# Performance work log

Measured on AMD Instinct MI355X. Metric: run time of the kernel, lower is better.

The kernel has to match this reference:

```python
import jax, jax.numpy as jnp
import numpy as np

# module config (mirrors init_kwargs)
D_MODEL = 1024
N_HEADS = 16
HEAD_DIM = D_MODEL // N_HEADS
WINDOW = 512
PREFIX = 16
B = 2
S = 4096  # divisible by WINDOW; S > WINDOW + PREFIX -> chunked windowed path


def setup_inputs() -> dict:
    key = jax.random.key(0)
    k1, k2, k3 = jax.random.split(key, 3)
    x = jax.random.normal(k1, (B, S, D_MODEL), dtype=jnp.float32)
    w_qkv = jax.random.normal(k2, (3 * D_MODEL, D_MODEL), dtype=jnp.float32) * 0.02
    w_out = jax.random.normal(k3, (D_MODEL, D_MODEL), dtype=jnp.float32) * 0.02
    return {"x": x, "w_qkv": w_qkv, "w_out": w_out}


def _windowed_global_attention(q, k, v):
    """q,k,v: [B,H,S,Dh]. Causal sliding-window (WINDOW) + global prefix (PREFIX) attention.
    Exactly matches torch's chunked SDPA: for query chunk starting at q_start, allowed keys are
    k_pos < PREFIX (causal) plus local keys in (q_pos-WINDOW, q_pos] with k_pos >= PREFIX."""
    Bb, H, S_, Dh = q.shape
    W, P = WINDOW, PREFIX
    C = S_ // W  # number of query chunks
    scale = 1.0 / np.sqrt(Dh).astype(np.float32)

    qc = q.reshape(Bb, H, C, W, Dh)  # [B,H,C,W,Dh]
    # pad W zero-keys at front so every chunk gathers a uniform 2W-key local tail
    kp = jnp.pad(k, ((0, 0), (0, 0), (W, 0), (0, 0)))
    vp = jnp.pad(v, ((0, 0), (0, 0), (W, 0), (0, 0)))
    tail_idx = jnp.arange(C)[:, None] * W + jnp.arange(2 * W)[None, :]  # [C,2W] (padded coords)
    kt = kp[:, :, tail_idx, :]  # [B,H,C,2W,Dh]
    vt = vp[:, :, tail_idx, :]
    kg = k[:, :, :P, :]  # global prefix keys [B,H,P,Dh]
    vg = v[:, :, :P, :]

    sg = jnp.einsum('bhcqd,bhkd->bhcqk', qc, kg) * scale   # [B,H,C,W,P]
    st = jnp.einsum('bhcqd,bhckd->bhcqk', qc, kt) * scale  # [B,H,C,W,2W]

    q_pos = jnp.arange(C)[:, None] * W + jnp.arange(W)[None, :]          # [C,W]
    kt_pos = jnp.arange(C)[:, None] * W - W + jnp.arange(2 * W)[None, :]  # [C,2W]
    # global prefix: causal only
    mg = jnp.arange(P)[None, None, :] <= q_pos[:, :, None]                # [C,W,P]
    # local tail: causal & within window & not already covered by global prefix (and not padding)
    diff = q_pos[:, :, None] - kt_pos[:, None, :]                          # [C,W,2W]
    mt = (diff >= 0) & (diff < W) & (kt_pos[:, None, :] >= P)

    neg = jnp.asarray(-1e9, sg.dtype)
    scores = jnp.concatenate([
        jnp.where(mg[None, None], sg, neg),
        jnp.where(mt[None, None], st, neg),
    ], axis=-1)  # [B,H,C,W,P+2W]
    attn = jax.nn.softmax(scores, axis=-1)

    vcat = jnp.concatenate([
        jnp.broadcast_to(vg[:, :, None], (Bb, H, C, P, Dh)), vt
    ], axis=3)  # [B,H,C,P+2W,Dh]
    out = jnp.einsum('bhcqk,bhckd->bhcqd', attn, vcat)
    return out.reshape(Bb, H, S_, Dh)


def reference(x, w_qkv, w_out):
    Bb, S_, Dm = x.shape
    qkv = x @ w_qkv.T                      # [B,S,3*Dm]
    q, k, v = jnp.split(qkv, 3, axis=-1)
    def heads(t):
        return t.reshape(Bb, S_, N_HEADS, HEAD_DIM).transpose(0, 2, 1, 3)
    q, k, v = heads(q), heads(k), heads(v)  # [B,H,S,Dh]
    o = _windowed_global_attention(q, k, v)
    o = o.transpose(0, 2, 1, 3).reshape(Bb, S_, Dm)
    return o @ w_out.T
```

## Files before the change

kernel.cpp:

```cpp
#include <hip/hip_runtime.h>
#include <hip/hip_bf16.h>

#define AS1 __attribute__((address_space(1)))
#define AS3 __attribute__((address_space(3)))

typedef unsigned short u16;
typedef short bf16x8 __attribute__((ext_vector_type(8)));
typedef unsigned short u16x8 __attribute__((ext_vector_type(8)));
typedef float f32x4 __attribute__((ext_vector_type(4)));

#define MFMA16 __builtin_amdgcn_mfma_f32_16x16x32_bf16


__device__ __forceinline__ u16 f2bf(float f) {
  union { float f; unsigned u; } c; c.f = f;
  unsigned u = c.u;
  u = u + 0x7fffu + ((u >> 16) & 1u);
  return (u16)(u >> 16);
}

__device__ __forceinline__ void gl_lds16(const void* g, void* l) {
  __builtin_amdgcn_global_load_lds((const AS1 void*)g, (AS3 void*)l, 16, 0, 0);
}

union fpu { float f; unsigned u; };


__global__ void cast_all_kernel(const float* __restrict__ x,
                                const float* __restrict__ wqkv,
                                const float* __restrict__ wout,
                                u16* __restrict__ ws) {
  int i = blockIdx.x * blockDim.x + threadIdx.x;
  const float4* src;
  int rel;
  size_t matbase;
  if (i < 2097152)      { src = (const float4*)x + i;                rel = i;           matbase = 0; }
  else if (i < 2883584) { src = (const float4*)wqkv + (i - 2097152); rel = i - 2097152; matbase = 8388608; }
  else                  { src = (const float4*)wout + (i - 2883584); rel = i - 2883584; matbase = 11534336; }
  float4 f = *src;
  ushort4 o;
  o.x = f2bf(f.x); o.y = f2bf(f.y); o.z = f2bf(f.z); o.w = f2bf(f.w);
  int fe  = rel * 4;
  int row = fe >> 10, c = fe & 1023;
  int newc = (c & ~63) | (((((c >> 3) ^ row) & 7) << 3)) | (c & 7);
  ((ushort4*)ws)[(matbase + (size_t)row * 1024 + newc) >> 2] = o;
}


template<int EPI>
__global__ __launch_bounds__(256) void gemm_bt(
    const u16* __restrict__ A, const u16* __restrict__ Bm,
    float* __restrict__ Cf,
    u16* __restrict__ qd, u16* __restrict__ kd, u16* __restrict__ vd,
    int M, int N, int K)
{
  __shared__ u16 As[128 * 64];
  __shared__ u16 Bs[128 * 64];

  const int tid  = threadIdx.x;
  const int wave = tid >> 6, lane = tid & 63;
  const int quad = lane >> 4, l16 = lane & 15;
  const int bm = blockIdx.y * 128, bn = blockIdx.x * 128;
  const int wm = (wave >> 1) * 64, wn = (wave & 1) * 64;

  f32x4 acc[4][4] = {};

  const int srow = wave * 32 + (lane >> 3);
  const int scol = (lane & 7) * 8;

  for (int kt = 0; kt < K; kt += 64) {
    __syncthreads();
    #pragma unroll
    for (int i = 0; i < 4; ++i) {
      gl_lds16(&A[(size_t)(bm + srow + i * 8) * K + kt + scol], &As[(wave * 32 + i * 8) * 64]);
      gl_lds16(&Bm[(size_t)(bn + srow + i * 8) * K + kt + scol], &Bs[(wave * 32 + i * 8) * 64]);
    }
    __syncthreads();
    #pragma unroll
    for (int kk = 0; kk < 64; kk += 32) {
      bf16x8 af[4], bb[4];
      #pragma unroll
      for (int i = 0; i < 4; ++i) {
        int row = wm + i * 16 + l16;
        af[i] = *(const bf16x8*)&As[row * 64 + (((((kk >> 3) + quad) ^ row) & 7) << 3)];
      }
      #pragma unroll
      for (int j = 0; j < 4; ++j) {
        int row = wn + j * 16 + l16;
        bb[j] = *(const bf16x8*)&Bs[row * 64 + (((((kk >> 3) + quad) ^ row) & 7) << 3)];
      }
      #pragma unroll
      for (int i = 0; i < 4; ++i)
        #pragma unroll
        for (int j = 0; j < 4; ++j)
          acc[i][j] = MFMA16(af[i], bb[j], acc[i][j], 0, 0, 0);
    }
  }

  #pragma unroll
  for (int i = 0; i < 4; ++i) {
    #pragma unroll
    for (int j = 0; j < 4; ++j) {
      #pragma unroll
      for (int r = 0; r < 4; ++r) {
        int m = bm + wm + i * 16 + quad * 4 + r;
        int n = bn + wn + j * 16 + l16;
        float val = acc[i][j][r];
        if (EPI == 0) {
          Cf[(size_t)m * N + n] = val;
        } else {
          int part = n >> 10, rem = n & 1023;
          int h = rem >> 6, d = rem & 63;
          int b = m >> 12, s = m & 4095;
          if (part == 0) val *= 0.1803368801111244f;
          u16* dst = (part == 0) ? qd : (part == 1) ? kd : vd;
          dst[((size_t)((b * 16 + h) * 4096 + s)) * 64 + d] = f2bf(val);
        }
      }
    }
  }
}


__global__ __launch_bounds__(256) void transpose_v(const u16* __restrict__ vb,
                                                   u16* __restrict__ vt) {
  __shared__ u16 Lt[64 * 72];
  const int tid = threadIdx.x, bid = blockIdx.x;
  const int bh = bid & 31, st = (bid >> 5) << 6;
  const size_t base = (size_t)bh << 18;
  #pragma unroll
  for (int c = 0; c < 2; ++c) {
    int idx = tid * 8 + c * 2048;
    int row = idx >> 6, col = idx & 63;
    u16x8 vv = *(const u16x8*)&vb[base + (size_t)(st + row) * 64 + col];
    #pragma unroll
    for (int s = 0; s < 8; ++s) Lt[(col + s) * 72 + row] = vv[s];
  }
  __syncthreads();
  #pragma unroll
  for (int c = 0; c < 2; ++c) {
    int d = (tid >> 3) + c * 32;
    int sg = (tid & 7) * 8;
    u16x8 o;
    #pragma unroll
    for (int s = 0; s < 8; ++s) o[s] = Lt[d * 72 + sg + s];
    *(u16x8*)&vt[base + (size_t)d * 4096 + st + sg] = o;
  }
}


__global__ __launch_bounds__(64) void attn_kernel(
    const u16* __restrict__ qb, const u16* __restrict__ kb,
    const u16* __restrict__ vt, u16* __restrict__ ob)
{
  __shared__ u16 Ps[32 * 64];

  const int lane = threadIdx.x;
  const int quad = lane >> 4, l16 = lane & 15;
  const int bid  = blockIdx.x;
  const int bh   = bid & 31;
  const int t0   = (bid >> 5) << 5;
  const size_t base = (size_t)bh << 18;

  bf16x8 bq[2][2];
  #pragma unroll
  for (int i = 0; i < 2; ++i) {
    const u16* qrow = qb + base + (size_t)(t0 + i * 16 + l16) * 64;
    bq[i][0] = *(const bf16x8*)(qrow + quad * 8);
    bq[i][1] = *(const bf16x8*)(qrow + 32 + quad * 8);
  }

  f32x4 oacc[2][4] = {};
  f32x4 lacc[2] = {};
  bf16x8 ones;
  #pragma unroll
  for (int s = 0; s < 8; ++s) ones[s] = (short)0x3F80;

  const int lo = max(0, t0 - 511) >> 6;
  const int hi = (t0 + 31) >> 6;

  auto loadK = [&](int kb0, bf16x8 (&kf)[4][2]) {
    #pragma unroll
    for (int j = 0; j < 4; ++j) {
      const u16* krow = kb + base + (size_t)(kb0 + j * 16 + l16) * 64;
      kf[j][0] = *(const bf16x8*)(krow + quad * 8);
      kf[j][1] = *(const bf16x8*)(krow + 32 + quad * 8);
    }
  };

  bf16x8 ka[4][2], kbuf2[4][2];

  {
    const u16* krow = kb + base + (size_t)l16 * 64;
    bf16x8 pk0 = *(const bf16x8*)(krow + quad * 8);
    bf16x8 pk1 = *(const bf16x8*)(krow + 32 + quad * 8);
    loadK(lo << 6, ka);

    #pragma unroll
    for (int i = 0; i < 2; ++i) {
      f32x4 t4 = {};
      t4 = MFMA16(pk0, bq[i][0], t4, 0, 0, 0);
      t4 = MFMA16(pk1, bq[i][1], t4, 0, 0, 0);
      int row = i * 16 + l16;
      int qpos = t0 + row;
      fpu p[4];
      #pragma unroll
      for (int r = 0; r < 4; ++r) {
        int kpos = quad * 4 + r;
        p[r].f = exp2f(kpos <= qpos ? t4[r] : -1e30f);
      }
      uint2 w;
      w.x = (p[1].u & 0xffff0000u) | (p[0].u >> 16);
      w.y = (p[3].u & 0xffff0000u) | (p[2].u >> 16);
      *(uint2*)&Ps[row * 64 + ((quad ^ l16) & 15) * 4] = w;
      uint2 z = {0u, 0u};
      *(uint2*)&Ps[row * 64 + (((4 + quad) ^ l16) & 15) * 4] = z;
    }
    #pragma unroll
    for (int i = 0; i < 2; ++i) {
      int row = i * 16 + l16;
      uint2 r0 = *(uint2*)&Ps[row * 64 + (((2 * quad) ^ l16) & 15) * 4];
      uint2 r1 = *(uint2*)&Ps[row * 64 + (((2 * quad + 1) ^ l16) & 15) * 4];
      union { uint4 u; bf16x8 v; } cc; cc.u = make_uint4(r0.x, r0.y, r1.x, r1.y);
      bf16x8 ap = cc.v;
      lacc[i] = MFMA16(ap, ones, lacc[i], 0, 0, 0);
      #pragma unroll
      for (int jd = 0; jd < 4; ++jd) {
        bf16x8 bv = *(const bf16x8*)&vt[base + (size_t)(jd * 16 + l16) * 4096 + quad * 8];
        oacc[i][jd] = MFMA16(ap, bv, oacc[i][jd], 0, 0, 0);
      }
    }
  }

  auto tilec = [&](int kb0, bf16x8 (&kf)[4][2]) {
    const bool full = (kb0 >= 16) && (kb0 + 63 <= t0) && (kb0 >= t0 + 31 - 511);
    #pragma unroll
    for (int j = 0; j < 4; ++j) {
      #pragma unroll
      for (int i = 0; i < 2; ++i) {
        f32x4 t4 = {};
        t4 = MFMA16(kf[j][0], bq[i][0], t4, 0, 0, 0);
        t4 = MFMA16(kf[j][1], bq[i][1], t4, 0, 0, 0);
        int row = i * 16 + l16;
        int qpos = t0 + row;
        fpu p[4];
        #pragma unroll
        for (int r = 0; r < 4; ++r) {
          float v = t4[r];
          if (!full) {
            int kpos = kb0 + j * 16 + quad * 4 + r;
            int diff = qpos - kpos;
            bool ok = (diff >= 0) && (diff < 512) && (kpos >= 16);
            v = ok ? v : -1e30f;
          }
          p[r].f = exp2f(v);
        }
        uint2 w;
        w.x = (p[1].u & 0xffff0000u) | (p[0].u >> 16);
        w.y = (p[3].u & 0xffff0000u) | (p[2].u >> 16);
        *(uint2*)&Ps[row * 64 + (((j * 4 + quad) ^ l16) & 15) * 4] = w;
      }
    }
    #pragma unroll
    for (int i = 0; i < 2; ++i) {
      int row = i * 16 + l16;
      #pragma unroll
      for (int h = 0; h < 2; ++h) {
        int g0 = h * 8 + 2 * quad;
        uint2 r0 = *(uint2*)&Ps[row * 64 + ((g0 ^ l16) & 15) * 4];
        uint2 r1 = *(uint2*)&Ps[row * 64 + (((g0 + 1) ^ l16) & 15) * 4];
        union { uint4 u; bf16x8 v; } cc; cc.u = make_uint4(r0.x, r0.y, r1.x, r1.y);
        bf16x8 ap = cc.v;
        lacc[i] = MFMA16(ap, ones, lacc[i], 0, 0, 0);
        #pragma unroll
        for (int jd = 0; jd < 4; ++jd) {
          bf16x8 bv = *(const bf16x8*)&vt[base + (size_t)(jd * 16 + l16) * 4096 + kb0 + h * 32 + quad * 8];
          oacc[i][jd] = MFMA16(ap, bv, oacc[i][jd], 0, 0, 0);
        }
      }
    }
  };

  for (int t = lo; t <= hi; t += 2) {
    if (t + 1 <= hi) loadK((t + 1) << 6, kbuf2);
    tilec(t << 6, ka);
    if (t + 1 <= hi) {
      if (t + 2 <= hi) loadK((t + 2) << 6, ka);
      tilec((t + 1) << 6, kbuf2);
    }
  }

  const int b = bh >> 4, h = bh & 15;
  #pragma unroll
  for (int i = 0; i < 2; ++i) {
    #pragma unroll
    for (int r = 0; r < 4; ++r) {
      float inv = 1.f / lacc[i][r];
      int srow = t0 + i * 16 + quad * 4 + r;
      size_t rowoff = ((size_t)(b * 4096 + srow)) * 1024 + h * 64;
      #pragma unroll
      for (int jd = 0; jd < 4; ++jd) {
        int g = ((jd * 2 + (l16 >> 3)) ^ srow) & 7;
        ob[rowoff + (g << 3) + (l16 & 7)] = f2bf(oacc[i][jd][r] * inv);
      }
    }
  }
}


extern "C" void kernel_launch(void* const* d_in, const int* in_sizes, int n_in,
                              void* d_out, int out_size, void* d_ws, size_t ws_size,
                              hipStream_t stream) {
  const float* x    = (const float*)d_in[0];
  const float* wqkv = (const float*)d_in[1];
  const float* wout = (const float*)d_in[2];
  float* out = (float*)d_out;

  u16* ws    = (u16*)d_ws;
  u16* xb    = ws;
  u16* wqkvb = xb + (size_t)8192 * 1024;
  u16* woutb = wqkvb + (size_t)3072 * 1024;
  u16* qbuf  = woutb + (size_t)1024 * 1024;
  u16* kbuf  = qbuf + (size_t)8388608;
  u16* vbuf  = kbuf + (size_t)8388608;
  u16* vtb   = vbuf + (size_t)8388608;
  u16* obuf  = xb;

  cast_all_kernel<<<12288, 256, 0, stream>>>(x, wqkv, wout, ws);

  gemm_bt<1><<<dim3(24, 64), 256, 0, stream>>>(xb, wqkvb, nullptr, qbuf, kbuf, vbuf,
                                               8192, 3072, 1024);
  transpose_v<<<2048, 256, 0, stream>>>(vbuf, vtb);
  attn_kernel<<<4096, 64, 0, stream>>>(qbuf, kbuf, vtb, obuf);
  gemm_bt<0><<<dim3(8, 64), 256, 0, stream>>>(obuf, woutb, out, nullptr, nullptr, nullptr,
                                              8192, 1024, 1024);
}
```

Baseline: 265.2 us.

## Pack four attention waves per block and prefetch V/K tiles in registers

The attention kernel now runs four independent waves per 256-thread block, each handling its own 32-query tile with a private LDS slice, in place of one 64-thread wave per block. The K/V loop is restructured to a single-tile loop that preloads the V fragments at the top of each iteration and prefetches the next K tile after the QK MFMAs, using precomputed pointers. Exp2 uses the hardware builtin, and bf16 packing uses a single perm instruction. This is meant to cut per-block launch overhead and hide global-load latency, at the cost of higher register pressure under the launch_bounds(256,3) occupancy target.

```diff
diff --git a/kernel.cpp b/kernel.cpp
--- a/kernel.cpp
+++ b/kernel.cpp
@@ -19,11 +19,22 @@
   return (u16)(u >> 16);
 }
 
+__device__ __forceinline__ float fexp2(float x) {
+#if __has_builtin(__builtin_amdgcn_exp2f)
+  return __builtin_amdgcn_exp2f(x);
+#else
+  return exp2f(x);
+#endif
+}
+
+__device__ __forceinline__ unsigned pack_bf(float a, float b) {
+  union { float f; unsigned u; } ua, ub; ua.f = a; ub.f = b;
+  return __builtin_amdgcn_perm(ub.u, ua.u, 0x07060302u);
+}
+
 __device__ __forceinline__ void gl_lds16(const void* g, void* l) {
   __builtin_amdgcn_global_load_lds((const AS1 void*)g, (AS3 void*)l, 16, 0, 0);
 }
-
-union fpu { float f; unsigned u; };
 
 
 __global__ void cast_all_kernel(const float* __restrict__ x,
@@ -149,26 +160,46 @@
 }
 
 
-__global__ __launch_bounds__(64) void attn_kernel(
+__global__ __launch_bounds__(256, 3) void attn_kernel(
     const u16* __restrict__ qb, const u16* __restrict__ kb,
     const u16* __restrict__ vt, u16* __restrict__ ob)
 {
-  __shared__ u16 Ps[32 * 64];
-
-  const int lane = threadIdx.x;
+  __shared__ u16 Ps[4][32 * 64];
+
+  const int tid  = threadIdx.x;
+  const int wave = tid >> 6;
+  const int lane = tid & 63;
   const int quad = lane >> 4, l16 = lane & 15;
   const int bid  = blockIdx.x;
   const int bh   = bid & 31;
-  const int t0   = (bid >> 5) << 5;
+  const int t0   = (((bid >> 5) << 2) | wave) << 5;
   const size_t base = (size_t)bh << 18;
-
-  bf16x8 bq[2][2];
-  #pragma unroll
-  for (int i = 0; i < 2; ++i) {
-    const u16* qrow = qb + base + (size_t)(t0 + i * 16 + l16) * 64;
-    bq[i][0] = *(const bf16x8*)(qrow + quad * 8);
-    bq[i][1] = *(const bf16x8*)(qrow + 32 + quad * 8);
-  }
+  u16* __restrict__ ps = &Ps[wave][0];
+
+  const int l64 = l16 * 64 + quad * 8;
+
+  const u16* qp = qb + base + (size_t)t0 * 64 + l64;
+  bf16x8 bq00 = *(const bf16x8*)(qp);
+  bf16x8 bq01 = *(const bf16x8*)(qp + 32);
+  bf16x8 bq10 = *(const bf16x8*)(qp + 1024);
+  bf16x8 bq11 = *(const bf16x8*)(qp + 1056);
+
+  const int lo = max(0, t0 - 511) >> 6;
+  const int hi = (t0 + 31) >> 6;
+
+  const u16* kp0 = kb + base + (size_t)(lo << 6) * 64 + l64;
+  const u16* kp2 = kp0 + 2048;
+  const u16* vq  = vt + base + (size_t)l16 * 4096 + quad * 8;
+  const u16* vp0 = vq + (lo << 6);
+  const u16* vp1 = vp0 + 65536;
+  const u16* vp2 = vp1 + 65536;
+  const u16* vp3 = vp2 + 65536;
+
+  bf16x8 kf[4][2];
+  kf[0][0] = *(const bf16x8*)(kp0);        kf[0][1] = *(const bf16x8*)(kp0 + 32);
+  kf[1][0] = *(const bf16x8*)(kp0 + 1024); kf[1][1] = *(const bf16x8*)(kp0 + 1056);
+  kf[2][0] = *(const bf16x8*)(kp2);        kf[2][1] = *(const bf16x8*)(kp2 + 32);
+  kf[3][0] = *(const bf16x8*)(kp2 + 1024); kf[3][1] = *(const bf16x8*)(kp2 + 1056);
 
   f32x4 oacc[2][4] = {};
   f32x4 lacc[2] = {};
@@ -176,118 +207,124 @@
   #pragma unroll
   for (int s = 0; s < 8; ++s) ones[s] = (short)0x3F80;
 
-  const int lo = max(0, t0 - 511) >> 6;
-  const int hi = (t0 + 31) >> 6;
-
-  auto loadK = [&](int kb0, bf16x8 (&kf)[4][2]) {
-    #pragma unroll
-    for (int j = 0; j < 4; ++j) {
-      const u16* krow = kb + base + (size_t)(kb0 + j * 16 + l16) * 64;
-      kf[j][0] = *(const bf16x8*)(krow + quad * 8);
-      kf[j][1] = *(const bf16x8*)(krow + 32 + quad * 8);
-    }
-  };
-
-  bf16x8 ka[4][2], kbuf2[4][2];
-
   {
-    const u16* krow = kb + base + (size_t)l16 * 64;
-    bf16x8 pk0 = *(const bf16x8*)(krow + quad * 8);
-    bf16x8 pk1 = *(const bf16x8*)(krow + 32 + quad * 8);
-    loadK(lo << 6, ka);
+    const u16* kpre = kb + base + l64;
+    bf16x8 pk0 = *(const bf16x8*)(kpre);
+    bf16x8 pk1 = *(const bf16x8*)(kpre + 32);
+    bf16x8 pv[4];
+    pv[0] = *(const bf16x8*)(vq);
+    pv[1] = *(const bf16x8*)(vq + 65536);
+    pv[2] = *(const bf16x8*)(vq + 131072);
+    pv[3] = *(const bf16x8*)(vq + 196608);
 
     #pragma unroll
     for (int i = 0; i < 2; ++i) {
       f32x4 t4 = {};
-      t4 = MFMA16(pk0, bq[i][0], t4, 0, 0, 0);
-      t4 = MFMA16(pk1, bq[i][1], t4, 0, 0, 0);
+      t4 = MFMA16(pk0, i ? bq10 : bq00, t4, 0, 0, 0);
+      t4 = MFMA16(pk1, i ? bq11 : bq01, t4, 0, 0, 0);
       int row = i * 16 + l16;
       int qpos = t0 + row;
-      fpu p[4];
+      float p[4];
       #pragma unroll
       for (int r = 0; r < 4; ++r) {
         int kpos = quad * 4 + r;
-        p[r].f = exp2f(kpos <= qpos ? t4[r] : -1e30f);
+        p[r] = fexp2(kpos <= qpos ? t4[r] : -1e30f);
       }
       uint2 w;
-      w.x = (p[1].u & 0xffff0000u) | (p[0].u >> 16);
-      w.y = (p[3].u & 0xffff0000u) | (p[2].u >> 16);
-      *(uint2*)&Ps[row * 64 + ((quad ^ l16) & 15) * 4] = w;
-      uint2 z = {0u, 0u};
-      *(uint2*)&Ps[row * 64 + (((4 + quad) ^ l16) & 15) * 4] = z;
+      w.x = pack_bf(p[0], p[1]);
+      w.y = pack_bf(p[2], p[3]);
+      *(uint2*)&ps[row * 64 + ((quad ^ l16) & 15) * 4] = w;
+      uint2 z; z.x = 0u; z.y = 0u;
+      *(uint2*)&ps[row * 64 + (((4 + quad) ^ l16) & 15) * 4] = z;
     }
     #pragma unroll
     for (int i = 0; i < 2; ++i) {
       int row = i * 16 + l16;
-      uint2 r0 = *(uint2*)&Ps[row * 64 + (((2 * quad) ^ l16) & 15) * 4];
-      uint2 r1 = *(uint2*)&Ps[row * 64 + (((2 * quad + 1) ^ l16) & 15) * 4];
+      uint2 r0 = *(uint2*)&ps[row * 64 + (((2 * quad) ^ l16) & 15) * 4];
+      uint2 r1 = *(uint2*)&ps[row * 64 + (((2 * quad + 1) ^ l16) & 15) * 4];
       union { uint4 u; bf16x8 v; } cc; cc.u = make_uint4(r0.x, r0.y, r1.x, r1.y);
       bf16x8 ap = cc.v;
       lacc[i] = MFMA16(ap, ones, lacc[i], 0, 0, 0);
       #pragma unroll
-      for (int jd = 0; jd < 4; ++jd) {
-        bf16x8 bv = *(const bf16x8*)&vt[base + (size_t)(jd * 16 + l16) * 4096 + quad * 8];
-        oacc[i][jd] = MFMA16(ap, bv, oacc[i][jd], 0, 0, 0);
-      }
-    }
-  }
-
-  auto tilec = [&](int kb0, bf16x8 (&kf)[4][2]) {
+      for (int jd = 0; jd < 4; ++jd)
+        oacc[i][jd] = MFMA16(ap, pv[jd], oacc[i][jd], 0, 0, 0);
+    }
+  }
+
+  for (int t = lo; t <= hi; ++t) {
+    const int kb0 = t << 6;
     const bool full = (kb0 >= 16) && (kb0 + 63 <= t0) && (kb0 >= t0 + 31 - 511);
+
+    bf16x8 bv[2][4];
+    bv[0][0] = *(const bf16x8*)(vp0);  bv[1][0] = *(const bf16x8*)(vp0 + 32);
+    bv[0][1] = *(const bf16x8*)(vp1);  bv[1][1] = *(const bf16x8*)(vp1 + 32);
+    bv[0][2] = *(const bf16x8*)(vp2);  bv[1][2] = *(const bf16x8*)(vp2 + 32);
+    bv[0][3] = *(const bf16x8*)(vp3);  bv[1][3] = *(const bf16x8*)(vp3 + 32);
+
+    f32x4 sc[4][2];
     #pragma unroll
     for (int j = 0; j < 4; ++j) {
       #pragma unroll
       for (int i = 0; i < 2; ++i) {
         f32x4 t4 = {};
-        t4 = MFMA16(kf[j][0], bq[i][0], t4, 0, 0, 0);
-        t4 = MFMA16(kf[j][1], bq[i][1], t4, 0, 0, 0);
+        t4 = MFMA16(kf[j][0], i ? bq10 : bq00, t4, 0, 0, 0);
+        t4 = MFMA16(kf[j][1], i ? bq11 : bq01, t4, 0, 0, 0);
+        sc[j][i] = t4;
+      }
+    }
+
+    if (t < hi) {
+      kp0 += 4096; kp2 += 4096;
+      kf[0][0] = *(const bf16x8*)(kp0);        kf[0][1] = *(const bf16x8*)(kp0 + 32);
+      kf[1][0] = *(const bf16x8*)(kp0 + 1024); kf[1][1] = *(const bf16x8*)(kp0 + 1056);
+      kf[2][0] = *(const bf16x8*)(kp2);        kf[2][1] = *(const bf16x8*)(kp2 + 32);
+      kf[3][0] = *(const bf16x8*)(kp2 + 1024); kf[3][1] = *(const bf16x8*)(kp2 + 1056);
+    }
+
+    #pragma unroll
+    for (int j = 0; j < 4; ++j) {
+      #pragma unroll
+      for (int i = 0; i < 2; ++i) {
         int row = i * 16 + l16;
-        int qpos = t0 + row;
-        fpu p[4];
-        #pragma unroll
-        for (int r = 0; r < 4; ++r) {
-          float v = t4[r];
-          if (!full) {
+        float p[4];
+        if (full) {
+          #pragma unroll
+          for (int r = 0; r < 4; ++r) p[r] = fexp2(sc[j][i][r]);
+        } else {
+          int qpos = t0 + row;
+          #pragma unroll
+          for (int r = 0; r < 4; ++r) {
             int kpos = kb0 + j * 16 + quad * 4 + r;
             int diff = qpos - kpos;
             bool ok = (diff >= 0) && (diff < 512) && (kpos >= 16);
-            v = ok ? v : -1e30f;
+            p[r] = fexp2(ok ? sc[j][i][r] : -1e30f);
           }
-          p[r].f = exp2f(v);
         }
         uint2 w;
-        w.x = (p[1].u & 0xffff0000u) | (p[0].u >> 16);
-        w.y = (p[3].u & 0xffff0000u) | (p[2].u >> 16);
-        *(uint2*)&Ps[row * 64 + (((j * 4 + quad) ^ l16) & 15) * 4] = w;
-      }
-    }
+        w.x = pack_bf(p[0], p[1]);
+        w.y = pack_bf(p[2], p[3]);
+        *(uint2*)&ps[row * 64 + (((j * 4 + quad) ^ l16) & 15) * 4] = w;
+      }
+    }
+
     #pragma unroll
     for (int i = 0; i < 2; ++i) {
       int row = i * 16 + l16;
       #pragma unroll
       for (int h = 0; h < 2; ++h) {
         int g0 = h * 8 + 2 * quad;
-        uint2 r0 = *(uint2*)&Ps[row * 64 + ((g0 ^ l16) & 15) * 4];
-        uint2 r1 = *(uint2*)&Ps[row * 64 + (((g0 + 1) ^ l16) & 15) * 4];
+        uint2 r0 = *(uint2*)&ps[row * 64 + ((g0 ^ l16) & 15) * 4];
+        uint2 r1 = *(uint2*)&ps[row * 64 + (((g0 + 1) ^ l16) & 15) * 4];
         union { uint4 u; bf16x8 v; } cc; cc.u = make_uint4(r0.x, r0.y, r1.x, r1.y);
         bf16x8 ap = cc.v;
         lacc[i] = MFMA16(ap, ones, lacc[i], 0, 0, 0);
         #pragma unroll
-        for (int jd = 0; jd < 4; ++jd) {
-          bf16x8 bv = *(const bf16x8*)&vt[base + (size_t)(jd * 16 + l16) * 4096 + kb0 + h * 32 + quad * 8];
-          oacc[i][jd] = MFMA16(ap, bv, oacc[i][jd], 0, 0, 0);
-        }
-      }
-    }
-  };
-
-  for (int t = lo; t <= hi; t += 2) {
-    if (t + 1 <= hi) loadK((t + 1) << 6, kbuf2);
-    tilec(t << 6, ka);
-    if (t + 1 <= hi) {
-      if (t + 2 <= hi) loadK((t + 2) << 6, ka);
-      tilec((t + 1) << 6, kbuf2);
-    }
+        for (int jd = 0; jd < 4; ++jd)
+          oacc[i][jd] = MFMA16(ap, bv[h][jd], oacc[i][jd], 0, 0, 0);
+      }
+    }
+
+    vp0 += 64; vp1 += 64; vp2 += 64; vp3 += 64;
   }
 
   const int b = bh >> 4, h = bh & 15;
@@ -331,7 +368,7 @@
   gemm_bt<1><<<dim3(24, 64), 256, 0, stream>>>(xb, wqkvb, nullptr, qbuf, kbuf, vbuf,
                                                8192, 3072, 1024);
   transpose_v<<<2048, 256, 0, stream>>>(vbuf, vtb);
-  attn_kernel<<<4096, 64, 0, stream>>>(qbuf, kbuf, vtb, obuf);
+  attn_kernel<<<1024, 256, 0, stream>>>(qbuf, kbuf, vtb, obuf);
   gemm_bt<0><<<dim3(8, 64), 256, 0, stream>>>(obuf, woutb, out, nullptr, nullptr, nullptr,
                                               8192, 1024, 1024);
 }
```

After: 334.4 us. 1.26x slower.
